# Performance work log

Measured on AMD Instinct MI355X. Metric: run time of the kernel, lower is better.

Reference implementation:

```python
import jax, jax.numpy as jnp
import numpy as np

B = 1024        # interactions per batch (graphs per side)
DIM = 64        # args.dim
HID = 64        # args.hidd_dim == args.word_dim
L = 2           # args.num_layers
NREL = 4        # relation types
N_USERS, N_ITEMS, N_WORDS = 100000, 50000, 50000
N = 131072      # total nodes per batched graph (per side)
E = 524288      # total edges per batched graph (per side)
D_FM = (L + 1) * DIM * 2  # 384


def setup_inputs() -> dict:
    key = jax.random.key(0)
    ks = iter(jax.random.split(key, 64))
    nrm = lambda shape, s=0.05: jax.random.normal(next(ks), shape, jnp.float32) * s
    ri = lambda shape, hi: jax.random.randint(next(ks), shape, 0, hi)
    # deterministic sorted graph-membership vector: equal-size graphs, no empty segments
    batch = (jnp.arange(N) * B) // N
    return dict(
        uid=ri((B,), N_USERS), iid=ri((B,), N_ITEMS),
        u_nodes=ri((N,), N_WORDS), i_nodes=ri((N,), N_WORDS),
        u_edge_index=ri((2, E), N), i_edge_index=ri((2, E), N),
        u_edge_type=ri((E,), NREL), i_edge_type=ri((E,), NREL),
        u_batch=batch, i_batch=batch,
        user_emb=nrm((N_USERS, DIM)), item_emb=nrm((N_ITEMS, DIM)), word_emb=nrm((N_WORDS, HID)),
        trans_u_W=nrm((L, DIM, HID)), trans_u_b=jnp.zeros((L, HID)),
        trans_i_W=nrm((L, DIM, HID)), trans_i_b=jnp.zeros((L, HID)),
        trans_w_W=nrm((L, HID, DIM)), trans_w_b=jnp.zeros((L, DIM)),
        inter_u_W=nrm((DIM, DIM)), inter_u_b=jnp.zeros((DIM,)),
        inter_i_W=nrm((DIM, DIM)), inter_i_b=jnp.zeros((DIM,)),
        conv_u_W=nrm((L, HID, HID)), conv_u_b=jnp.zeros((L, HID)),
        conv_u_att=nrm((L, 3, HID)), conv_u_rel=nrm((L, NREL, HID)),
        conv_i_W=nrm((L, HID, HID)), conv_i_b=jnp.zeros((L, HID)),
        conv_i_att=nrm((L, 3, HID)), conv_i_rel=nrm((L, NREL, HID)),
        pool_W=nrm((HID, HID)),
        fm_w=nrm((D_FM,)), fm_V=nrm((D_FM, D_FM)),
        fm_bias_u=jnp.zeros((N_USERS,)), fm_bias_i=jnp.zeros((N_ITEMS,)), fm_bias=jnp.zeros((1,)),
    )


def _gat(x, ei, et, W, b, att, rel):
    """Relational GAT conv: attention over incoming edges with relation-type term."""
    n = x.shape[0]
    h = x @ W + b                         # [n, HID]
    src, dst = ei[0], ei[1]
    e = jax.nn.leaky_relu(h[src] @ att[0] + h[dst] @ att[1] + rel[et] @ att[2], 0.2)  # [E]
    emax = jax.ops.segment_max(e, dst, num_segments=n)
    emax = jnp.where(jnp.isfinite(emax), emax, 0.0)   # guard nodes with no in-edges
    ex = jnp.exp(e - emax[dst])
    den = jax.ops.segment_sum(ex, dst, num_segments=n)
    alpha = ex / (den[dst] + 1e-16)
    return jax.nn.relu(jax.ops.segment_sum(alpha[:, None] * h[src], dst, num_segments=n))


def _conv_pool(ui_em, x, ei, et, batch, Ws, bs, atts, rels, tw_W, tw_b, pool_W, nb):
    """L stages of GAT conv -> query-conditioned soft pooling gate -> global max pool."""
    inv_sqrt_d = 1.0 / np.sqrt(HID).astype(np.float32)
    outs = []
    for i in range(L):
        x = _gat(x, ei, et, Ws[i], bs[i], atts[i], rels[i])
        q = ui_em[i]                                          # [B, HID] per-graph query
        score = jax.nn.sigmoid(jnp.sum((x @ pool_W) * q[batch], -1) * inv_sqrt_d)  # [N]
        x = x * score[:, None]
        pooled = jax.ops.segment_max(x, batch, num_segments=nb)  # gmp -> [B, HID]
        outs.append(jax.nn.relu(pooled @ tw_W[i] + tw_b[i]))     # trans_w -> [B, DIM]
    return jnp.concatenate(outs, -1)                             # [B, L*DIM]


def reference(uid, iid, u_nodes, i_nodes, u_edge_index, i_edge_index,
              u_edge_type, i_edge_type, u_batch, i_batch,
              user_emb, item_emb, word_emb,
              trans_u_W, trans_u_b, trans_i_W, trans_i_b, trans_w_W, trans_w_b,
              inter_u_W, inter_u_b, inter_i_W, inter_i_b,
              conv_u_W, conv_u_b, conv_u_att, conv_u_rel,
              conv_i_W, conv_i_b, conv_i_att, conv_i_rel,
              pool_W, fm_w, fm_V, fm_bias_u, fm_bias_i, fm_bias):
    u_e = user_emb[uid]                                        # [B, DIM]
    i_e = item_emb[iid]
    u_em = [jax.nn.relu(u_e @ trans_u_W[i] + trans_u_b[i]) for i in range(L)]
    i_em = [jax.nn.relu(i_e @ trans_i_W[i] + trans_i_b[i]) for i in range(L)]
    u_pool = _conv_pool(u_em, word_emb[u_nodes], u_edge_index, u_edge_type, u_batch,
                        conv_u_W, conv_u_b, conv_u_att, conv_u_rel,
                        trans_w_W, trans_w_b, pool_W, B)
    i_pool = _conv_pool(i_em, word_emb[i_nodes], i_edge_index, i_edge_type, i_batch,
                        conv_i_W, conv_i_b, conv_i_att, conv_i_rel,
                        trans_w_W, trans_w_b, pool_W, B)
    user_rep = jax.nn.relu(u_e @ inter_u_W + inter_u_b)
    item_rep = jax.nn.relu(i_e @ inter_i_W + inter_i_b)
    x = jnp.concatenate([user_rep, u_pool, item_rep, i_pool], -1)   # [B, D_FM]
    # FM layer (degree-2 interaction with full V matrix, as in source)
    linear = x @ fm_w                                               # [B]
    xv = x @ fm_V                                                   # [B, D_FM]
    mlp = 0.5 * jnp.sum(xv * xv - (x * x) @ (fm_V * fm_V), -1)
    return linear + mlp + fm_bias_u[uid] + fm_bias_i[iid] + fm_bias[0]
```

## Files before the change

kernel.cpp:

```cpp
#include <hip/hip_runtime.h>
#include <hip/hip_bf16.h>

#define NN 131072
#define NE 524288
#define NB 1024

typedef __attribute__((ext_vector_type(8))) short short8;
typedef __attribute__((ext_vector_type(4))) float f32x4;

__device__ __forceinline__ float wsum(float v){
#pragma unroll
  for (int o = 32; o > 0; o >>= 1) v += __shfl_xor(v, o, 64);
  return v;
}
__device__ __forceinline__ short f2bs(float f){
  __hip_bfloat16 t = __float2bfloat16(f);
  union { __hip_bfloat16 b; short s; } u; u.b = t; return u.s;
}
__device__ __forceinline__ float bs2f(short s){
  return __uint_as_float(((unsigned)(unsigned short)s) << 16);
}
__device__ __forceinline__ float ulo2f(unsigned v){ return __uint_as_float(v << 16); }
__device__ __forceinline__ float uhi2f(unsigned v){ return __uint_as_float(v & 0xFFFF0000u); }
__device__ __forceinline__ unsigned fpack(float x, float y){
  return (unsigned)(unsigned short)f2bs(x) | ((unsigned)(unsigned short)f2bs(y) << 16);
}

__global__ void k_mega(int wconvB,
                       const int* __restrict__ u_ei, const int* __restrict__ i_ei,
                       int* __restrict__ cnt, int* __restrict__ loff,
                       const float* __restrict__ wemb, unsigned* __restrict__ wtab,
                       int n32,
                       const float* __restrict__ cuW, const float* __restrict__ ciW,
                       const float* __restrict__ pW,
                       const float* __restrict__ cub, const float* __restrict__ cib,
                       const float* __restrict__ uatt, const float* __restrict__ iatt,
                       const float* __restrict__ urel, const float* __restrict__ irel,
                       short8* __restrict__ frag, float* __restrict__ waA,
                       float* __restrict__ ba, float* __restrict__ rtab,
                       const int* __restrict__ uid, const int* __restrict__ iid,
                       const float* __restrict__ uemb, const float* __restrict__ iemb,
                       const float* __restrict__ uiW, const float* __restrict__ uib,
                       const float* __restrict__ iiW, const float* __restrict__ iib,
                       const float* __restrict__ utW, const float* __restrict__ utb,
                       const float* __restrict__ itW, const float* __restrict__ itb,
                       float* __restrict__ xfm, float* __restrict__ q){
  const int histB = 2 * NE / 256;
  int blk = blockIdx.x, tid = threadIdx.x;
  if (blk < histB){
    int ee = blk * 256 + tid;
    int side = ee >= NE;
    int e = ee - side * NE;
    const int* ei = side ? i_ei : u_ei;
    int dst = ei[NE + e] + side * NN;
    int p = atomicAdd(&cnt[dst << 2], 1);
    loff[ee] = p;
  } else if (blk < histB + 10){
    int b2 = blk - histB;
    int mat = b2 >> 1;
    const float* W = mat < 2 ? cuW + mat * 4096 : (mat < 4 ? ciW + (mat - 2) * 4096 : pW);
    int g = (b2 & 1) * 256 + tid;
    int lane = g & 63, rest = g >> 6;
    int hh = rest & 1, t = rest >> 1;
    int m = lane & 15, qq = lane >> 4;
    short8 v;
#pragma unroll
    for (int j = 0; j < 8; j++)
      v[j] = f2bs(W[(hh * 32 + qq * 8 + j) * 64 + (t * 16 + m)]);
    frag[mat * 512 + g] = v;
  } else if (blk < histB + 12){
    int side = blk - histB - 10;
    const float* W    = side ? ciW : cuW;
    const float* bias = side ? cib : cub;
    const float* att  = side ? iatt : uatt;
    const float* rel  = side ? irel : urel;
    int l = tid >> 7, a = (tid >> 6) & 1, kk = tid & 63;
    float s = 0.f;
    for (int c = 0; c < 64; c++) s += W[l * 4096 + kk * 64 + c] * att[l * 192 + a * 64 + c];
    waA[((side * 2 + l) * 2 + a) * 64 + kk] = s;
    if (tid < 4){
      int l2 = tid >> 1, a2 = tid & 1;
      float sb = 0.f;
      for (int c = 0; c < 64; c++) sb += bias[l2 * 64 + c] * att[l2 * 192 + a2 * 64 + c];
      ba[(side * 2 + l2) * 2 + a2] = sb;
    }
    if (tid >= 4 && tid < 12){
      int id = tid - 4, l2 = id >> 2, tt = id & 3;
      float sr = 0.f;
      for (int c = 0; c < 64; c++) sr += rel[l2 * 256 + tt * 64 + c] * att[l2 * 192 + 128 + c];
      rtab[(side * 2 + l2) * 4 + tt] = sr;
    }
  } else if (blk < histB + 12 + wconvB){
    int id = (blk - histB - 12) * 256 + tid;
    if (id < n32){
      const float2* src = (const float2*)wemb;
      float2 v = src[id];
      wtab[id] = fpack(v.x, v.y);
    }
  } else {
    int lane = tid & 63, w = tid >> 6;
    int b = (blk - histB - 12 - wconvB) * 4 + w;
    int side = b >= NB;
    int lb = b - side * NB;
    const int* ids = side ? iid : uid;
    const float* emb = side ? iemb : uemb;
    const float* interW = side ? iiW : uiW;
    const float* interB = side ? iib : uib;
    const float* transW = side ? itW : utW;
    const float* transB = side ? itb : utb;
    int repOff = side ? 192 : 0;
    float xe = emb[(long)ids[lb] * 64 + lane];
    float o = interB[lane];
#pragma unroll
    for (int k = 0; k < 64; k++) o += __shfl(xe, k, 64) * interW[k * 64 + lane];
    xfm[lb * 384 + repOff + lane] = fmaxf(o, 0.f);
    for (int l = 0; l < 2; l++){
      float t = transB[l * 64 + lane];
#pragma unroll
      for (int k = 0; k < 64; k++) t += __shfl(xe, k, 64) * transW[l * 4096 + k * 64 + lane];
      q[((size_t)(side * 2 + l) * NB + lb) * 64 + lane] = fmaxf(t, 0.f);
    }
  }
}

__global__ void k_scan1(const int* __restrict__ cnt, int* __restrict__ rowptr,
                        int* __restrict__ bsum){
  __shared__ int sh[256];
  int i = blockIdx.x * 256 + threadIdx.x;
  int v = cnt[i << 2];
  sh[threadIdx.x] = v; __syncthreads();
  for (int off = 1; off < 256; off <<= 1){
    int t = (threadIdx.x >= off) ? sh[threadIdx.x - off] : 0;
    __syncthreads();
    sh[threadIdx.x] += t;
    __syncthreads();
  }
  int incl = sh[threadIdx.x];
  rowptr[i] = incl - v;
  if (threadIdx.x == 255) bsum[blockIdx.x] = incl;
}

__global__ void k_scan2(int* __restrict__ bsum){
  __shared__ int sh[1024];
  int v = bsum[threadIdx.x];
  sh[threadIdx.x] = v; __syncthreads();
  for (int off = 1; off < 1024; off <<= 1){
    int t = (threadIdx.x >= off) ? sh[threadIdx.x - off] : 0;
    __syncthreads();
    sh[threadIdx.x] += t;
    __syncthreads();
  }
  bsum[threadIdx.x] = sh[threadIdx.x] - v;
}

__global__ void k_scw(const int* __restrict__ u_ei, const int* __restrict__ i_ei,
                      const int* __restrict__ u_et, const int* __restrict__ i_et,
                      const int* __restrict__ rowptr, const int* __restrict__ bsum,
                      const int* __restrict__ loff, int* __restrict__ pedge,
                      int* __restrict__ rowfin,
                      const short* __restrict__ wtab, int nwords, int wgB,
                      const float* __restrict__ waA, const float* __restrict__ ba,
                      float* __restrict__ wa0, float* __restrict__ wa1){
  const int scatB = 2 * NE / 256;
  int blk = blockIdx.x, tid = threadIdx.x;
  if (blk < scatB){
    int ee = blk * 256 + tid;
    int side = ee >= NE;
    int e = ee - side * NE;
    const int* ei = side ? i_ei : u_ei;
    const int* et = side ? i_et : u_et;
    int dst = ei[NE + e] + side * NN;
    int src = ei[e] + side * NN;
    int p = rowptr[dst] + bsum[dst >> 8] + loff[ee];
    pedge[p] = src | (et[e] << 18);
  } else if (blk < scatB + wgB){
    int lane = tid & 63, w = tid >> 6;
    int q = lane >> 4, cl = lane & 15;
    int sw0 = ((blk - scatB) * 4 + w) * 8;
    const uint2* wt2 = (const uint2*)wtab;
    for (int it = 0; it < 2; it++){
      int wj = sw0 + it * 4 + q;
      if (wj >= 2 * nwords) continue;
      int side = wj >= nwords;
      int wid = wj - side * nwords;
      const float* A0 = waA + (side * 2 + 0) * 2 * 64;
      const float* A1 = A0 + 64;
      uint2 v = wt2[(long)wid * 16 + cl];
      int d = 4 * cl;
      float p0 = ulo2f(v.x) * A0[d] + uhi2f(v.x) * A0[d + 1] +
                 ulo2f(v.y) * A0[d + 2] + uhi2f(v.y) * A0[d + 3];
      float p1 = ulo2f(v.x) * A1[d] + uhi2f(v.x) * A1[d + 1] +
                 ulo2f(v.y) * A1[d + 2] + uhi2f(v.y) * A1[d + 3];
      p0 += __shfl_xor(p0, 1, 64); p0 += __shfl_xor(p0, 2, 64);
      p0 += __shfl_xor(p0, 4, 64); p0 += __shfl_xor(p0, 8, 64);
      p1 += __shfl_xor(p1, 1, 64); p1 += __shfl_xor(p1, 2, 64);
      p1 += __shfl_xor(p1, 4, 64); p1 += __shfl_xor(p1, 8, 64);
      if (cl == 0){
        wa0[(size_t)side * nwords + wid] = p0 + ba[side * 4 + 0];
        wa1[(size_t)side * nwords + wid] = p1 + ba[side * 4 + 1];
      }
    }
  } else {
    int i = (blk - scatB - wgB) * 256 + tid;
    rowfin[i] = rowptr[i] + bsum[i >> 8];
    if (i == 0) rowfin[2 * NN] = 2 * NE;
  }
}

template<int L>
__device__ __forceinline__ void dev_agg(
    const int* __restrict__ rowptr, const int* __restrict__ pedge,
    const float* __restrict__ a0, const float* __restrict__ a1,
    const float* __restrict__ wa0, const float* __restrict__ wa1,
    const int* __restrict__ u_nodes, const int* __restrict__ i_nodes, int nwords,
    const float* __restrict__ rtab, const short* __restrict__ rows,
    unsigned* __restrict__ xo32){
  int lane = threadIdx.x & 63, w = threadIdx.x >> 6;
  int grp = lane >> 4, cl = lane & 15;
  int nb = (blockIdx.x * 4 + w) * 8;
  int side = nb >= NN;
  const float* rt = rtab + (side * 2 + L) * 4;
  float rt0 = rt[0], rt1 = rt[1], rt2 = rt[2], rt3 = rt[3];
  const int* nodesS = side ? i_nodes : u_nodes;
  const float* wa0S = wa0 + (size_t)side * nwords;
  const float* wa1S = wa1 + (size_t)side * nwords;
  const uint2* h2 = (const uint2*)rows;

  for (int t = 0; t < 2; t++){
    int n = nb + grp * 2 + t;
    int r0 = rowptr[n], r1 = rowptr[n + 1];
    int deg = r1 - r0;
    float a1n;
    if (L == 0) a1n = wa1S[nodesS[n - side * NN]];
    else        a1n = a1[n];

    int pe[8]; int rowv[8]; float av[8]; uint2 hv[8];
#pragma unroll
    for (int j = 0; j < 8; j++)
      pe[j] = (j < deg) ? pedge[r0 + j] : 0;
#pragma unroll
    for (int j = 0; j < 8; j++){
      int s = pe[j] & 0x3FFFF;
      if (L == 0){
        int wid = 0;
        if (j < deg) wid = nodesS[s - side * NN];
        rowv[j] = wid;
      } else {
        rowv[j] = s;
      }
    }
#pragma unroll
    for (int j = 0; j < 8; j++){
      av[j] = 0.f;
      if (j < deg) av[j] = (L == 0) ? wa0S[rowv[j]] : a0[rowv[j]];
      uint2 z; z.x = 0u; z.y = 0u;
      hv[j] = z;
      if (j < deg) hv[j] = h2[(long)rowv[j] * 16 + cl];
    }
    float ax0 = 0.f, ay0 = 0.f, ax1 = 0.f, ay1 = 0.f, den = 0.f;
#pragma unroll
    for (int j = 0; j < 8; j++){
      int et = (pe[j] >> 18) & 3;
      float rr = (et & 2) ? ((et & 1) ? rt3 : rt2) : ((et & 1) ? rt1 : rt0);
      float v = av[j] + a1n + rr;
      v = (v > 0.f) ? v : 0.2f * v;
      float ex = (j < deg) ? __expf(v) : 0.f;
      ax0 += ex * ulo2f(hv[j].x); ay0 += ex * uhi2f(hv[j].x);
      ax1 += ex * ulo2f(hv[j].y); ay1 += ex * uhi2f(hv[j].y);
      den += ex;
    }
    for (int e = r0 + 8; e < r1; ++e){
      int pe2 = pedge[e];
      int s = pe2 & 0x3FFFF;
      int et = (pe2 >> 18) & 3;
      float rr = (et & 2) ? ((et & 1) ? rt3 : rt2) : ((et & 1) ? rt1 : rt0);
      float avv; long row;
      if (L == 0){ int wid = nodesS[s - side * NN]; avv = wa0S[wid]; row = wid; }
      else       { avv = a0[s]; row = s; }
      float v = avv + a1n + rr;
      v = (v > 0.f) ? v : 0.2f * v;
      float ex = __expf(v);
      uint2 hvv = h2[row * 16 + cl];
      ax0 += ex * ulo2f(hvv.x); ay0 += ex * uhi2f(hvv.x);
      ax1 += ex * ulo2f(hvv.y); ay1 += ex * uhi2f(hvv.y);
      den += ex;
    }
    float inv = 1.f / (den + 1e-16f);
    uint2 o;
    o.x = fpack(ax0 * inv, ay0 * inv);
    o.y = fpack(ax1 * inv, ay1 * inv);
    ((uint2*)xo32)[(long)n * 16 + cl] = o;
  }
}

__global__ __launch_bounds__(256) void k_agg0(
    const int* __restrict__ rowptr, const int* __restrict__ pedge,
    const float* __restrict__ wa0, const float* __restrict__ wa1,
    const int* __restrict__ u_nodes, const int* __restrict__ i_nodes, int nwords,
    const float* __restrict__ rtab, const short* __restrict__ wtab,
    unsigned* __restrict__ xo32){
  dev_agg<0>(rowptr, pedge, nullptr, nullptr, wa0, wa1, u_nodes, i_nodes, nwords,
             rtab, wtab, xo32);
}

__global__ __launch_bounds__(256) void k_agg1(
    const int* __restrict__ rowptr, const int* __restrict__ pedge,
    const float* __restrict__ a0, const float* __restrict__ a1,
    const float* __restrict__ rtab, const short* __restrict__ x,
    unsigned* __restrict__ xo32){
  dev_agg<1>(rowptr, pedge, a0, a1, nullptr, nullptr, nullptr, nullptr, 0,
             rtab, x, xo32);
}

__global__ __launch_bounds__(256) void k_gp(
    int l, const short* __restrict__ xagg, const short8* __restrict__ frag,
    const float* __restrict__ cub, const float* __restrict__ cib,
    const float* __restrict__ waA_all, const float* __restrict__ ba_all,
    const float* __restrict__ qbuf, const float* __restrict__ twW_all,
    const float* __restrict__ twb_all, float* __restrict__ xfm,
    short* __restrict__ xnext, float* __restrict__ a0, float* __restrict__ a1){
  __shared__ short xt[128 * 72];
  __shared__ float gates[128];
  __shared__ float red[4][64];
  int b = blockIdx.x;
  int side = b >= NB;
  int g = b - side * NB;
  long base = (long)side * NN + (long)g * 128;
  int tid = threadIdx.x, lane = tid & 63, w = tid >> 6;
  int m = lane & 15, q = lane >> 4;
  const short8* wfrag = frag + (side * 2 + l) * 512;
  const float* bias = (side ? cib : cub) + l * 64;
  short8 Bf[4][2];
#pragma unroll
  for (int t = 0; t < 4; t++)
#pragma unroll
    for (int hh = 0; hh < 2; hh++)
      Bf[t][hh] = wfrag[(t * 2 + hh) * 64 + lane];
  float bs[4];
#pragma unroll
  for (int t = 0; t < 4; t++) bs[t] = bias[t * 16 + m];
  f32x4 accA[2][4];
#pragma unroll
  for (int rb = 0; rb < 2; rb++){
    long n0 = base + w * 32 + rb * 16;
    const short8* xr = (const short8*)(xagg + (n0 + m) * 64);
    short8 A0 = xr[q];
    short8 A1 = xr[q + 4];
#pragma unroll
    for (int t = 0; t < 4; t++){
      f32x4 acc = (f32x4){bs[t], bs[t], bs[t], bs[t]};
      acc = __builtin_amdgcn_mfma_f32_16x16x32_bf16(A0, Bf[t][0], acc, 0, 0, 0);
      acc = __builtin_amdgcn_mfma_f32_16x16x32_bf16(A1, Bf[t][1], acc, 0, 0, 0);
#pragma unroll
      for (int r = 0; r < 4; r++) acc[r] = fmaxf(acc[r], 0.f);
      accA[rb][t] = acc;
#pragma unroll
      for (int r = 0; r < 4; r++)
        xt[(w * 32 + rb * 16 + q * 4 + r) * 72 + t * 16 + m] = f2bs(acc[r]);
    }
  }
  __syncthreads();
  const short8* pfrag = frag + 4 * 512;
  const float* qv_ = qbuf + ((size_t)(side * 2 + l) * NB + g) * 64;
  short8 Pf[4][2];
#pragma unroll
  for (int t = 0; t < 4; t++)
#pragma unroll
    for (int hh = 0; hh < 2; hh++)
      Pf[t][hh] = pfrag[(t * 2 + hh) * 64 + lane];
  float qv[4];
#pragma unroll
  for (int t = 0; t < 4; t++) qv[t] = qv_[t * 16 + m];
#pragma unroll
  for (int rb = 0; rb < 2; rb++){
    int rowb = w * 32 + rb * 16;
    short8 A0 = *(const short8*)(xt + (rowb + m) * 72 + q * 8);
    short8 A1 = *(const short8*)(xt + (rowb + m) * 72 + 32 + q * 8);
    f32x4 accp[4];
#pragma unroll
    for (int t = 0; t < 4; t++){
      accp[t] = (f32x4){0.f, 0.f, 0.f, 0.f};
      accp[t] = __builtin_amdgcn_mfma_f32_16x16x32_bf16(A0, Pf[t][0], accp[t], 0, 0, 0);
      accp[t] = __builtin_amdgcn_mfma_f32_16x16x32_bf16(A1, Pf[t][1], accp[t], 0, 0, 0);
    }
#pragma unroll
    for (int r = 0; r < 4; r++){
      float p = accp[0][r] * qv[0] + accp[1][r] * qv[1] +
                accp[2][r] * qv[2] + accp[3][r] * qv[3];
      p += __shfl_xor(p, 1, 64); p += __shfl_xor(p, 2, 64);
      p += __shfl_xor(p, 4, 64); p += __shfl_xor(p, 8, 64);
      if (m == 0)
        gates[rowb + q * 4 + r] = 1.f / (1.f + __expf(-p * 0.125f));
    }
  }
  __syncthreads();
  const unsigned* xt32 = (const unsigned*)xt;
  int c = lane & 31, half = lane >> 5;
  float mxx = 0.f, mxy = 0.f;
#pragma unroll
  for (int p = 0; p < 16; p++){
    int nn = w * 32 + 2 * p + half;
    unsigned v = xt32[nn * 36 + c];
    float gt = gates[nn];
    mxx = fmaxf(mxx, ulo2f(v) * gt);
    mxy = fmaxf(mxy, uhi2f(v) * gt);
  }
  mxx = fmaxf(mxx, __shfl_xor(mxx, 32, 64));
  mxy = fmaxf(mxy, __shfl_xor(mxy, 32, 64));
  if (half == 0){ red[w][2 * c] = mxx; red[w][2 * c + 1] = mxy; }
  __syncthreads();
  if (tid < 64){
    const float* twW = twW_all + l * 4096;
    const float* twb = twb_all + l * 64;
    int off = (side ? 256 : 64) + l * 64;
    float p = fmaxf(fmaxf(red[0][tid], red[1][tid]), fmaxf(red[2][tid], red[3][tid]));
    float o = twb[tid];
    red[0][tid] = p;
    __syncwarp();
    for (int d = 0; d < 64; d++) o += red[0][d] * twW[d * 64 + tid];
    xfm[g * 384 + off + tid] = fmaxf(o, 0.f);
  }
  if (l == 0){
#pragma unroll
    for (int p = 0; p < 4; p++){
      int row = p * 32 + (tid >> 3);
      int col8 = (tid & 7) * 8;
      float gt = gates[row];
      short8 v = *(const short8*)(xt + row * 72 + col8);
      short8 o;
#pragma unroll
      for (int j = 0; j < 8; j++) o[j] = f2bs(bs2f(v[j]) * gt);
      *(short8*)(xnext + (base + row) * 64 + col8) = o;
    }
    const float* wn0p = waA_all + ((side * 2 + 1) * 2 + 0) * 64;
    const float* wn1p = wn0p + 64;
    float wn0[4], wn1[4];
#pragma unroll
    for (int t = 0; t < 4; t++){ wn0[t] = wn0p[t * 16 + m]; wn1[t] = wn1p[t * 16 + m]; }
    float ban0 = ba_all[(side * 2 + 1) * 2 + 0];
    float ban1 = ba_all[(side * 2 + 1) * 2 + 1];
#pragma unroll
    for (int rb = 0; rb < 2; rb++)
#pragma unroll
      for (int r = 0; r < 4; r++){
        float p0 = accA[rb][0][r] * wn0[0] + accA[rb][1][r] * wn0[1] +
                   accA[rb][2][r] * wn0[2] + accA[rb][3][r] * wn0[3];
        float p1 = accA[rb][0][r] * wn1[0] + accA[rb][1][r] * wn1[1] +
                   accA[rb][2][r] * wn1[2] + accA[rb][3][r] * wn1[3];
        p0 += __shfl_xor(p0, 1, 64); p0 += __shfl_xor(p0, 2, 64);
        p0 += __shfl_xor(p0, 4, 64); p0 += __shfl_xor(p0, 8, 64);
        p1 += __shfl_xor(p1, 1, 64); p1 += __shfl_xor(p1, 2, 64);
        p1 += __shfl_xor(p1, 4, 64); p1 += __shfl_xor(p1, 8, 64);
        if (m == 0){
          int row = w * 32 + rb * 16 + q * 4 + r;
          float gr = gates[row];
          a0[base + row] = p0 * gr + ban0;
          a1[base + row] = p1 * gr + ban1;
        }
      }
  }
}

__global__ __launch_bounds__(384) void k_fm(
    const float* __restrict__ xfm, const float* __restrict__ V,
    const float* __restrict__ fw, const float* __restrict__ bu,
    const float* __restrict__ bi, const float* __restrict__ b0,
    const int* __restrict__ uid, const int* __restrict__ iid,
    float* __restrict__ out){
  __shared__ float xsh[4][384];
  __shared__ float xsq[4][384];
  __shared__ float part[4][384];
  int j = threadIdx.x;
  int g0 = blockIdx.x * 4;
#pragma unroll
  for (int b = 0; b < 4; b++){
    float xv_ = xfm[(g0 + b) * 384 + j];
    xsh[b][j] = xv_;
    xsq[b][j] = xv_ * xv_;
  }
  __syncthreads();
  float xv[4] = {0.f, 0.f, 0.f, 0.f};
  float vv[4] = {0.f, 0.f, 0.f, 0.f};
  for (int k = 0; k < 384; k++){
    float v = V[(size_t)k * 384 + j];
    float v2 = v * v;
#pragma unroll
    for (int b = 0; b < 4; b++){
      xv[b] = fmaf(xsh[b][k], v, xv[b]);
      vv[b] = fmaf(xsq[b][k], v2, vv[b]);
    }
  }
  float fwj = fw[j];
#pragma unroll
  for (int b = 0; b < 4; b++)
    part[b][j] = 0.5f * (xv[b] * xv[b] - vv[b]) + xsh[b][j] * fwj;
  __syncthreads();
  int w = j >> 6, lane = j & 63;
  if (w < 4){
    float s = part[w][lane] + part[w][lane + 64] + part[w][lane + 128] +
              part[w][lane + 192] + part[w][lane + 256] + part[w][lane + 320];
    s = wsum(s);
    if (lane == 0){
      int b = g0 + w;
      out[b] = s + bu[uid[b]] + bi[iid[b]] + b0[0];
    }
  }
}

extern "C" void kernel_launch(void* const* d_in, const int* in_sizes, int n_in,
                              void* d_out, int out_size, void* d_ws, size_t ws_size,
                              hipStream_t stream) {
  const int* uid      = (const int*)d_in[0];
  const int* iid      = (const int*)d_in[1];
  const int* u_nodes  = (const int*)d_in[2];
  const int* i_nodes  = (const int*)d_in[3];
  const int* u_ei     = (const int*)d_in[4];
  const int* i_ei     = (const int*)d_in[5];
  const int* u_et     = (const int*)d_in[6];
  const int* i_et     = (const int*)d_in[7];
  const float* user_emb = (const float*)d_in[10];
  const float* item_emb = (const float*)d_in[11];
  const float* word_emb = (const float*)d_in[12];
  const float* trans_u_W = (const float*)d_in[13];
  const float* trans_u_b = (const float*)d_in[14];
  const float* trans_i_W = (const float*)d_in[15];
  const float* trans_i_b = (const float*)d_in[16];
  const float* trans_w_W = (const float*)d_in[17];
  const float* trans_w_b = (const float*)d_in[18];
  const float* inter_u_W = (const float*)d_in[19];
  const float* inter_u_b = (const float*)d_in[20];
  const float* inter_i_W = (const float*)d_in[21];
  const float* inter_i_b = (const float*)d_in[22];
  const float* conv_u_W  = (const float*)d_in[23];
  const float* conv_u_b  = (const float*)d_in[24];
  const float* conv_u_att= (const float*)d_in[25];
  const float* conv_u_rel= (const float*)d_in[26];
  const float* conv_i_W  = (const float*)d_in[27];
  const float* conv_i_b  = (const float*)d_in[28];
  const float* conv_i_att= (const float*)d_in[29];
  const float* conv_i_rel= (const float*)d_in[30];
  const float* pool_W    = (const float*)d_in[31];
  const float* fm_w      = (const float*)d_in[32];
  const float* fm_V      = (const float*)d_in[33];
  const float* fm_bias_u = (const float*)d_in[34];
  const float* fm_bias_i = (const float*)d_in[35];
  const float* fm_bias   = (const float*)d_in[36];
  float* out = (float*)d_out;
  int n32 = in_sizes[12] / 2;
  int nwords = in_sizes[12] / 64;
  int wconvB = (n32 + 255) / 256;

  char* w = (char*)d_ws;
  short* X0   = (short*)w;          w += (size_t)2 * NN * 64 * 2;
  short* X1   = (short*)w;          w += (size_t)2 * NN * 64 * 2;
  short* wtab = (short*)w;          w += (size_t)in_sizes[12] * 2;
  int* pedge  = (int*)w;            w += (size_t)2 * NE * 4;
  float* a0   = (float*)w;          w += (size_t)2 * NN * 4;
  float* a1   = (float*)w;          w += (size_t)2 * NN * 4;
  float* wa0  = (float*)w;          w += (size_t)2 * nwords * 4;
  float* wa1  = (float*)w;          w += (size_t)2 * nwords * 4;
  int* rowptr = (int*)w;            w += (size_t)2 * NN * 4;
  int* rowfin = (int*)w;            w += (size_t)(2 * NN + 256) * 4;
  int* bsum   = (int*)w;            w += 1024 * 4;
  short8* frag = (short8*)w;        w += (size_t)5 * 512 * 16;
  float* waA  = (float*)w;          w += 2 * 2 * 2 * 64 * 4;
  float* ba   = (float*)w;          w += 64;
  float* rtab = (float*)w;          w += 64;
  float* qbuf = (float*)w;          w += (size_t)4 * NB * 64 * 4;
  float* xfm  = (float*)w;          w += (size_t)NB * 384 * 4;
  int* cnt  = (int*)X1;
  int* loff = (int*)X0;

  hipMemsetAsync(cnt, 0, (size_t)2 * NN * 16, stream);

  int histB = 2 * NE / 256;
  int megaB = histB + 12 + wconvB + 2 * NB / 4;
  k_mega<<<megaB, 256, 0, stream>>>(wconvB, u_ei, i_ei, cnt, loff,
                                    word_emb, (unsigned*)wtab, n32,
                                    conv_u_W, conv_i_W, pool_W, conv_u_b, conv_i_b,
                                    conv_u_att, conv_i_att, conv_u_rel, conv_i_rel,
                                    frag, waA, ba, rtab,
                                    uid, iid, user_emb, item_emb,
                                    inter_u_W, inter_u_b, inter_i_W, inter_i_b,
                                    trans_u_W, trans_u_b, trans_i_W, trans_i_b,
                                    xfm, qbuf);
  k_scan1<<<2 * NN / 256, 256, 0, stream>>>(cnt, rowptr, bsum);
  k_scan2<<<1, 1024, 0, stream>>>(bsum);
  int wgB = (2 * nwords + 31) / 32;
  int scatB = 2 * NE / 256;
  int finB = 2 * NN / 256;
  k_scw<<<scatB + wgB + finB, 256, 0, stream>>>(u_ei, i_ei, u_et, i_et,
                                                rowptr, bsum, loff, pedge, rowfin,
                                                wtab, nwords, wgB, waA, ba, wa0, wa1);

  k_agg0<<<2 * NN / 32, 256, 0, stream>>>(rowfin, pedge, wa0, wa1,
                                          u_nodes, i_nodes, nwords, rtab,
                                          wtab, (unsigned*)X0);
  k_gp  <<<2 * NB, 256, 0, stream>>>(0, X0, frag, conv_u_b, conv_i_b, waA, ba,
                                     qbuf, trans_w_W, trans_w_b, xfm, X1, a0, a1);
  k_agg1<<<2 * NN / 32, 256, 0, stream>>>(rowfin, pedge, a0, a1, rtab,
                                          X1, (unsigned*)X0);
  k_gp  <<<2 * NB, 256, 0, stream>>>(1, X0, frag, conv_u_b, conv_i_b, waA, ba,
                                     qbuf, trans_w_W, trans_w_b, xfm,
                                     nullptr, nullptr, nullptr);

  k_fm<<<NB / 4, 384, 0, stream>>>(xfm, fm_V, fm_w, fm_bias_u, fm_bias_i, fm_bias,
                                   uid, iid, out);
}
```

Baseline: 414.4 us.

## Build CSR via two-pass bucketed radix sort with shared-memory histograms

Replaces the global-atomic per-node edge counting, two-level node scan and random scatter with a bucketed counting sort. Edges are first histogrammed into 512 coarse destination buckets in shared memory, column-scanned, and scattered into bucket order. A per-bucket kernel then does a local histogram and scan to produce row pointers and the final sorted edge list. This removes the memset and global atomics in exchange for an extra pass over the edges and an extra kernel launch. It also assumes src fits in 18 bits and type in 2 bits so the local dst index can be packed above them.

```diff
diff --git a/kernel.cpp b/kernel.cpp
--- a/kernel.cpp
+++ b/kernel.cpp
@@ -4,6 +4,8 @@
 #define NN 131072
 #define NE 524288
 #define NB 1024
+#define NBKT 512
+#define K1B 512
 
 typedef __attribute__((ext_vector_type(8))) short short8;
 typedef __attribute__((ext_vector_type(4))) float f32x4;
@@ -28,7 +30,7 @@
 
 __global__ void k_mega(int wconvB,
                        const int* __restrict__ u_ei, const int* __restrict__ i_ei,
-                       int* __restrict__ cnt, int* __restrict__ loff,
+                       int* __restrict__ cntmat,
                        const float* __restrict__ wemb, unsigned* __restrict__ wtab,
                        int n32,
                        const float* __restrict__ cuW, const float* __restrict__ ciW,
@@ -45,18 +47,25 @@
                        const float* __restrict__ utW, const float* __restrict__ utb,
                        const float* __restrict__ itW, const float* __restrict__ itb,
                        float* __restrict__ xfm, float* __restrict__ q){
-  const int histB = 2 * NE / 256;
   int blk = blockIdx.x, tid = threadIdx.x;
-  if (blk < histB){
-    int ee = blk * 256 + tid;
-    int side = ee >= NE;
-    int e = ee - side * NE;
-    const int* ei = side ? i_ei : u_ei;
-    int dst = ei[NE + e] + side * NN;
-    int p = atomicAdd(&cnt[dst << 2], 1);
-    loff[ee] = p;
-  } else if (blk < histB + 10){
-    int b2 = blk - histB;
+  if (blk < K1B){
+    __shared__ int hist[NBKT];
+    hist[tid] = 0; hist[tid + 256] = 0;
+    __syncthreads();
+#pragma unroll
+    for (int k = 0; k < 8; k++){
+      int ee = blk * 2048 + k * 256 + tid;
+      int side = ee >= NE;
+      int e = ee - side * NE;
+      const int* ei = side ? i_ei : u_ei;
+      int dst = ei[NE + e] + side * NN;
+      atomicAdd(&hist[dst >> 9], 1);
+    }
+    __syncthreads();
+    cntmat[blk * NBKT + tid] = hist[tid];
+    cntmat[blk * NBKT + tid + 256] = hist[tid + 256];
+  } else if (blk < K1B + 10){
+    int b2 = blk - K1B;
     int mat = b2 >> 1;
     const float* W = mat < 2 ? cuW + mat * 4096 : (mat < 4 ? ciW + (mat - 2) * 4096 : pW);
     int g = (b2 & 1) * 256 + tid;
@@ -68,8 +77,8 @@
     for (int j = 0; j < 8; j++)
       v[j] = f2bs(W[(hh * 32 + qq * 8 + j) * 64 + (t * 16 + m)]);
     frag[mat * 512 + g] = v;
-  } else if (blk < histB + 12){
-    int side = blk - histB - 10;
+  } else if (blk < K1B + 12){
+    int side = blk - K1B - 10;
     const float* W    = side ? ciW : cuW;
     const float* bias = side ? cib : cub;
     const float* att  = side ? iatt : uatt;
@@ -90,8 +99,8 @@
       for (int c = 0; c < 64; c++) sr += rel[l2 * 256 + tt * 64 + c] * att[l2 * 192 + 128 + c];
       rtab[(side * 2 + l2) * 4 + tt] = sr;
     }
-  } else if (blk < histB + 12 + wconvB){
-    int id = (blk - histB - 12) * 256 + tid;
+  } else if (blk < K1B + 12 + wconvB){
+    int id = (blk - K1B - 12) * 256 + tid;
     if (id < n32){
       const float2* src = (const float2*)wemb;
       float2 v = src[id];
@@ -99,7 +108,7 @@
     }
   } else {
     int lane = tid & 63, w = tid >> 6;
-    int b = (blk - histB - 12 - wconvB) * 4 + w;
+    int b = (blk - K1B - 12 - wconvB) * 4 + w;
     int side = b >= NB;
     int lb = b - side * NB;
     const int* ids = side ? iid : uid;
@@ -123,60 +132,73 @@
   }
 }
 
-__global__ void k_scan1(const int* __restrict__ cnt, int* __restrict__ rowptr,
-                        int* __restrict__ bsum){
+__global__ void k_colscan(int* __restrict__ cntmat, int* __restrict__ btot){
   __shared__ int sh[256];
-  int i = blockIdx.x * 256 + threadIdx.x;
-  int v = cnt[i << 2];
-  sh[threadIdx.x] = v; __syncthreads();
+  int b = blockIdx.x, t = threadIdx.x;
+  int c0 = cntmat[(2 * t) * NBKT + b];
+  int c1 = cntmat[(2 * t + 1) * NBKT + b];
+  int s = c0 + c1;
+  sh[t] = s; __syncthreads();
   for (int off = 1; off < 256; off <<= 1){
-    int t = (threadIdx.x >= off) ? sh[threadIdx.x - off] : 0;
-    __syncthreads();
-    sh[threadIdx.x] += t;
-    __syncthreads();
-  }
-  int incl = sh[threadIdx.x];
-  rowptr[i] = incl - v;
-  if (threadIdx.x == 255) bsum[blockIdx.x] = incl;
-}
-
-__global__ void k_scan2(int* __restrict__ bsum){
-  __shared__ int sh[1024];
-  int v = bsum[threadIdx.x];
-  sh[threadIdx.x] = v; __syncthreads();
-  for (int off = 1; off < 1024; off <<= 1){
-    int t = (threadIdx.x >= off) ? sh[threadIdx.x - off] : 0;
-    __syncthreads();
-    sh[threadIdx.x] += t;
-    __syncthreads();
-  }
-  bsum[threadIdx.x] = sh[threadIdx.x] - v;
-}
-
-__global__ void k_scw(const int* __restrict__ u_ei, const int* __restrict__ i_ei,
-                      const int* __restrict__ u_et, const int* __restrict__ i_et,
-                      const int* __restrict__ rowptr, const int* __restrict__ bsum,
-                      const int* __restrict__ loff, int* __restrict__ pedge,
-                      int* __restrict__ rowfin,
-                      const short* __restrict__ wtab, int nwords, int wgB,
-                      const float* __restrict__ waA, const float* __restrict__ ba,
-                      float* __restrict__ wa0, float* __restrict__ wa1){
-  const int scatB = 2 * NE / 256;
+    int v = (t >= off) ? sh[t - off] : 0;
+    __syncthreads();
+    sh[t] += v;
+    __syncthreads();
+  }
+  int incl = sh[t];
+  int excl = incl - s;
+  cntmat[(2 * t) * NBKT + b] = excl;
+  cntmat[(2 * t + 1) * NBKT + b] = excl + c0;
+  if (t == 255) btot[b] = incl;
+}
+
+__global__ void k_bscan(const int* __restrict__ btot, int* __restrict__ bbase){
+  __shared__ int sh[NBKT];
+  int t = threadIdx.x;
+  int v = btot[t];
+  sh[t] = v; __syncthreads();
+  for (int off = 1; off < NBKT; off <<= 1){
+    int x = (t >= off) ? sh[t - off] : 0;
+    __syncthreads();
+    sh[t] += x;
+    __syncthreads();
+  }
+  bbase[t] = sh[t] - v;
+  if (t == NBKT - 1) bbase[NBKT] = 2 * NE;
+}
+
+__global__ void k_scat(const int* __restrict__ u_ei, const int* __restrict__ i_ei,
+                       const int* __restrict__ u_et, const int* __restrict__ i_et,
+                       const int* __restrict__ cntmat, const int* __restrict__ bbase,
+                       int* __restrict__ ebuf,
+                       const short* __restrict__ wtab, int nwords,
+                       const float* __restrict__ waA, const float* __restrict__ ba,
+                       float* __restrict__ wa0, float* __restrict__ wa1){
   int blk = blockIdx.x, tid = threadIdx.x;
-  if (blk < scatB){
-    int ee = blk * 256 + tid;
-    int side = ee >= NE;
-    int e = ee - side * NE;
-    const int* ei = side ? i_ei : u_ei;
-    const int* et = side ? i_et : u_et;
-    int dst = ei[NE + e] + side * NN;
-    int src = ei[e] + side * NN;
-    int p = rowptr[dst] + bsum[dst >> 8] + loff[ee];
-    pedge[p] = src | (et[e] << 18);
-  } else if (blk < scatB + wgB){
+  if (blk < K1B){
+    __shared__ int hist[NBKT];
+    __shared__ int mb[NBKT];
+    hist[tid] = 0; hist[tid + 256] = 0;
+    mb[tid]       = cntmat[blk * NBKT + tid]       + bbase[tid];
+    mb[tid + 256] = cntmat[blk * NBKT + tid + 256] + bbase[tid + 256];
+    __syncthreads();
+#pragma unroll
+    for (int k = 0; k < 8; k++){
+      int ee = blk * 2048 + k * 256 + tid;
+      int side = ee >= NE;
+      int e = ee - side * NE;
+      const int* ei = side ? i_ei : u_ei;
+      const int* et = side ? i_et : u_et;
+      int dst = ei[NE + e] + side * NN;
+      int src = ei[e] + side * NN;
+      int bin = dst >> 9;
+      int slot = atomicAdd(&hist[bin], 1);
+      ebuf[mb[bin] + slot] = src | (et[e] << 18) | ((dst & 511) << 20);
+    }
+  } else {
     int lane = tid & 63, w = tid >> 6;
     int q = lane >> 4, cl = lane & 15;
-    int sw0 = ((blk - scatB) * 4 + w) * 8;
+    int sw0 = ((blk - K1B) * 4 + w) * 8;
     const uint2* wt2 = (const uint2*)wtab;
     for (int it = 0; it < 2; it++){
       int wj = sw0 + it * 4 + q;
@@ -200,11 +222,44 @@
         wa1[(size_t)side * nwords + wid] = p1 + ba[side * 4 + 1];
       }
     }
-  } else {
-    int i = (blk - scatB - wgB) * 256 + tid;
-    rowfin[i] = rowptr[i] + bsum[i >> 8];
-    if (i == 0) rowfin[2 * NN] = 2 * NE;
-  }
+  }
+}
+
+__global__ __launch_bounds__(256) void k_csr(
+    const int* __restrict__ bbase, const int* __restrict__ ebuf,
+    int* __restrict__ rowfin, int* __restrict__ pedge){
+  __shared__ int hist[NBKT];
+  __shared__ int sh[256];
+  int b = blockIdx.x, t = threadIdx.x;
+  int eb0 = bbase[b], eb1 = bbase[b + 1];
+  hist[t] = 0; hist[t + 256] = 0;
+  __syncthreads();
+  for (int e = eb0 + t; e < eb1; e += 256)
+    atomicAdd(&hist[(ebuf[e] >> 20) & 511], 1);
+  __syncthreads();
+  int c0 = hist[2 * t], c1 = hist[2 * t + 1];
+  int s = c0 + c1;
+  sh[t] = s; __syncthreads();
+  for (int off = 1; off < 256; off <<= 1){
+    int v = (t >= off) ? sh[t - off] : 0;
+    __syncthreads();
+    sh[t] += v;
+    __syncthreads();
+  }
+  int excl = sh[t] - s;
+  int nbase = b * 512;
+  rowfin[nbase + 2 * t] = eb0 + excl;
+  rowfin[nbase + 2 * t + 1] = eb0 + excl + c0;
+  hist[2 * t] = excl;
+  hist[2 * t + 1] = excl + c0;
+  __syncthreads();
+  for (int e = eb0 + t; e < eb1; e += 256){
+    int rec = ebuf[e];
+    int bin = (rec >> 20) & 511;
+    int p = atomicAdd(&hist[bin], 1);
+    pedge[eb0 + p] = rec & 0xFFFFF;
+  }
+  if (b == NBKT - 1 && t == 0) rowfin[2 * NN] = 2 * NE;
 }
 
 template<int L>
@@ -559,23 +614,20 @@
   float* a1   = (float*)w;          w += (size_t)2 * NN * 4;
   float* wa0  = (float*)w;          w += (size_t)2 * nwords * 4;
   float* wa1  = (float*)w;          w += (size_t)2 * nwords * 4;
-  int* rowptr = (int*)w;            w += (size_t)2 * NN * 4;
+  int* cntmat = (int*)w;            w += (size_t)K1B * NBKT * 4;
   int* rowfin = (int*)w;            w += (size_t)(2 * NN + 256) * 4;
-  int* bsum   = (int*)w;            w += 1024 * 4;
+  int* btot   = (int*)w;            w += NBKT * 4;
+  int* bbase  = (int*)w;            w += (NBKT + 1) * 4;
   short8* frag = (short8*)w;        w += (size_t)5 * 512 * 16;
   float* waA  = (float*)w;          w += 2 * 2 * 2 * 64 * 4;
   float* ba   = (float*)w;          w += 64;
   float* rtab = (float*)w;          w += 64;
   float* qbuf = (float*)w;          w += (size_t)4 * NB * 64 * 4;
   float* xfm  = (float*)w;          w += (size_t)NB * 384 * 4;
-  int* cnt  = (int*)X1;
-  int* loff = (int*)X0;
-
-  hipMemsetAsync(cnt, 0, (size_t)2 * NN * 16, stream);
-
-  int histB = 2 * NE / 256;
-  int megaB = histB + 12 + wconvB + 2 * NB / 4;
-  k_mega<<<megaB, 256, 0, stream>>>(wconvB, u_ei, i_ei, cnt, loff,
+  int* ebuf = (int*)X0;
+
+  int megaB = K1B + 12 + wconvB + 2 * NB / 4;
+  k_mega<<<megaB, 256, 0, stream>>>(wconvB, u_ei, i_ei, cntmat,
                                     word_emb, (unsigned*)wtab, n32,
                                     conv_u_W, conv_i_W, pool_W, conv_u_b, conv_i_b,
                                     conv_u_att, conv_i_att, conv_u_rel, conv_i_rel,
@@ -584,14 +636,12 @@
                                     inter_u_W, inter_u_b, inter_i_W, inter_i_b,
                                     trans_u_W, trans_u_b, trans_i_W, trans_i_b,
                                     xfm, qbuf);
-  k_scan1<<<2 * NN / 256, 256, 0, stream>>>(cnt, rowptr, bsum);
-  k_scan2<<<1, 1024, 0, stream>>>(bsum);
+  k_colscan<<<NBKT, 256, 0, stream>>>(cntmat, btot);
+  k_bscan<<<1, NBKT, 0, stream>>>(btot, bbase);
   int wgB = (2 * nwords + 31) / 32;
-  int scatB = 2 * NE / 256;
-  int finB = 2 * NN / 256;
-  k_scw<<<scatB + wgB + finB, 256, 0, stream>>>(u_ei, i_ei, u_et, i_et,
-                                                rowptr, bsum, loff, pedge, rowfin,
-                                                wtab, nwords, wgB, waA, ba, wa0, wa1);
+  k_scat<<<K1B + wgB, 256, 0, stream>>>(u_ei, i_ei, u_et, i_et, cntmat, bbase,
+                                        ebuf, wtab, nwords, waA, ba, wa0, wa1);
+  k_csr<<<NBKT, 256, 0, stream>>>(bbase, ebuf, rowfin, pedge);
 
   k_agg0<<<2 * NN / 32, 256, 0, stream>>>(rowfin, pedge, wa0, wa1,
                                           u_nodes, i_nodes, nwords, rtab,
```

After: 374.6 us. -9.6%, faster.
